# Optimization experiments

Hardware: AMD Instinct MI355X
Metric: run time of the kernel (lower is better)

## Reference

```python
import jax, jax.numpy as jnp
import numpy as np

N_NODES = 100000
N_EDGES = 1600000
IN_CH = 128
HID = 64
HEADS = 4
N_GRAPHS = 64
NEG_SLOPE = 0.2
LN_EPS = 1e-5


def setup_inputs() -> dict:
    key = jax.random.key(0)
    ks = jax.random.split(key, 24)
    C1 = HID // HEADS  # 16 per-head channels for conv1
    inp = {
        "x": jax.random.normal(ks[0], (N_NODES, IN_CH), dtype=jnp.float32),
        "edge_index": jax.random.randint(ks[1], (2, N_EDGES), 0, N_NODES, dtype=jnp.int64),
        "batch": jnp.sort(jax.random.randint(ks[2], (N_NODES,), 0, N_GRAPHS, dtype=jnp.int64)),
        "num_graphs": N_GRAPHS,
        # conv1: GATConv(IN_CH -> C1, heads=HEADS, concat)
        "W1": jax.random.normal(ks[3], (IN_CH, HEADS * C1), dtype=jnp.float32) * 0.05,
        "att_src1": jax.random.normal(ks[4], (HEADS, C1), dtype=jnp.float32) * 0.1,
        "att_dst1": jax.random.normal(ks[5], (HEADS, C1), dtype=jnp.float32) * 0.1,
        "b1": jnp.zeros((HEADS * C1,), dtype=jnp.float32),
        # conv2: GATConv(HID -> HID, heads=1)
        "W2": jax.random.normal(ks[6], (HID, HID), dtype=jnp.float32) * 0.1,
        "att_src2": jax.random.normal(ks[7], (1, HID), dtype=jnp.float32) * 0.1,
        "att_dst2": jax.random.normal(ks[8], (1, HID), dtype=jnp.float32) * 0.1,
        "b2": jnp.zeros((HID,), dtype=jnp.float32),
        "ln_g": jnp.ones((HID,), dtype=jnp.float32),
        "ln_b": jnp.zeros((HID,), dtype=jnp.float32),
        "w_pool": jax.random.normal(ks[9], (HID, 1), dtype=jnp.float32) * 0.1,
        "b_pool": jnp.zeros((1,), dtype=jnp.float32),
        "w_fc1": jax.random.normal(ks[10], (HID, HID), dtype=jnp.float32) * 0.1,
        "b_fc1": jnp.zeros((HID,), dtype=jnp.float32),
        "w_fc2": jax.random.normal(ks[11], (HID, 1), dtype=jnp.float32) * 0.1,
        "b_fc2": jnp.zeros((1,), dtype=jnp.float32),
    }
    return inp


def gat_conv(x, src, dst, n_nodes, W, att_src, att_dst, bias, heads, out_ch):
    """PyG GATConv (add_self_loops already folded into src/dst)."""
    h = (x @ W).reshape(n_nodes, heads, out_ch)         # [N,H,C]
    a_s = jnp.sum(h * att_src[None], axis=-1)           # [N,H]
    a_d = jnp.sum(h * att_dst[None], axis=-1)           # [N,H]
    alpha = jax.nn.leaky_relu(a_s[src] + a_d[dst], NEG_SLOPE)  # [E,H]
    amax = jax.ops.segment_max(alpha, dst, num_segments=n_nodes)
    amax = jnp.where(jnp.isfinite(amax), amax, 0.0)
    ex = jnp.exp(alpha - amax[dst])
    denom = jax.ops.segment_sum(ex, dst, num_segments=n_nodes)
    w = ex / (denom[dst] + 1e-16)                       # segment softmax over in-edges
    msg = h[src] * w[:, :, None]                        # [E,H,C]
    out = jax.ops.segment_sum(msg, dst, num_segments=n_nodes)
    return out.reshape(n_nodes, heads * out_ch) + bias


def reference(x, edge_index, batch, num_graphs, W1, att_src1, att_dst1, b1,
              W2, att_src2, att_dst2, b2, ln_g, ln_b, w_pool, b_pool,
              w_fc1, b_fc1, w_fc2, b_fc2):
    n = x.shape[0]
    loop = jnp.arange(n, dtype=edge_index.dtype)
    src = jnp.concatenate([edge_index[0], loop])
    dst = jnp.concatenate([edge_index[1], loop])

    h = gat_conv(x, src, dst, n, W1, att_src1, att_dst1, b1, HEADS, HID // HEADS)
    h = jax.nn.elu(h)                                   # dropout is identity in eval
    h_res = h
    h = gat_conv(h, src, dst, n, W2, att_src2, att_dst2, b2, 1, HID)
    h = h + h_res
    mu = jnp.mean(h, axis=-1, keepdims=True)
    var = jnp.mean(jnp.square(h - mu), axis=-1, keepdims=True)
    h = (h - mu) / jnp.sqrt(var + LN_EPS) * ln_g + ln_b
    h = jax.nn.elu(h)

    attn = jax.nn.softmax(h @ w_pool + b_pool, axis=0)  # softmax over ALL nodes (dim=0)
    pooled = jax.ops.segment_sum(h * attn, batch, num_segments=num_graphs)  # [G,HID]
    z = jax.nn.elu(pooled @ w_fc1 + b_fc1)
    return z @ w_fc2 + b_fc2                            # [G,1]
```

## Files before the change

kernel.cpp:

```cpp
#include <hip/hip_runtime.h>
#include <math.h>

#define NN 100000
#define NE 1600000
#define ICH 128
#define HID 64
#define NGR 64
#define NB_SCAN 391

__device__ __forceinline__ float lrelu(float x){ return x > 0.f ? x : 0.2f*x; }
__device__ __forceinline__ float eluf(float x){ return x > 0.f ? x : expm1f(x); }

__device__ __forceinline__ float bf2f(unsigned short u){
  return __uint_as_float(((unsigned int)u) << 16);
}
__device__ __forceinline__ unsigned short f2bf(float f){
  unsigned int u = __float_as_uint(f);
  return (unsigned short)((u + 0x7FFF + ((u >> 16) & 1)) >> 16);
}

__device__ __forceinline__ float wsum64(float v){
  #pragma unroll
  for (int m = 32; m >= 1; m >>= 1) v += __shfl_xor(v, m);
  return v;
}
__device__ __forceinline__ float wsum16(float v){
  v += __shfl_xor(v, 8); v += __shfl_xor(v, 4);
  v += __shfl_xor(v, 2); v += __shfl_xor(v, 1);
  return v;
}
__device__ __forceinline__ int wscan_incl(int v){
  const int lane = threadIdx.x & 63;
  #pragma unroll
  for (int d = 1; d < 64; d <<= 1){
    int t = __shfl_up(v, d);
    if (lane >= d) v += t;
  }
  return v;
}

__global__ __launch_bounds__(256) void k_deg(const int* __restrict__ ei_dst,
                                             int* __restrict__ deg)
{
  const int lo = (blockIdx.x & 3) * 25000, hi = lo + 25000;
  const int nb = gridDim.x >> 2, ib = blockIdx.x >> 2;
  for (int e = ib * 256 + threadIdx.x; e < NE; e += nb * 256){
    int d = ei_dst[e];
    if (d >= lo && d < hi) atomicAdd(&deg[d], 1);
  }
}

__global__ __launch_bounds__(256) void k_scanA(const int* __restrict__ deg,
    int* __restrict__ rowptr, int* __restrict__ bsum)
{
  int i = blockIdx.x * 256 + threadIdx.x;
  int v = (i < NN) ? deg[i] : 0;
  int incl = wscan_incl(v);
  __shared__ int wsums[4];
  int w = threadIdx.x >> 6, lane = threadIdx.x & 63;
  if (lane == 63) wsums[w] = incl;
  __syncthreads();
  int off = 0;
  for (int k = 0; k < w; ++k) off += wsums[k];
  if (i < NN) rowptr[i] = incl - v + off;
  if (threadIdx.x == 255) bsum[blockIdx.x] = off + incl;
}

__global__ __launch_bounds__(512) void k_scanB(const int* __restrict__ bsum,
                                               int* __restrict__ boff)
{
  int i = threadIdx.x;
  int v = (i < NB_SCAN) ? bsum[i] : 0;
  int incl = wscan_incl(v);
  __shared__ int wsums[8];
  int w = threadIdx.x >> 6, lane = threadIdx.x & 63;
  if (lane == 63) wsums[w] = incl;
  __syncthreads();
  int off = 0;
  for (int k = 0; k < w; ++k) off += wsums[k];
  if (i < NB_SCAN) boff[i] = incl - v + off;
}

__global__ __launch_bounds__(256) void k_scanC(int* __restrict__ rowptr,
    const int* __restrict__ boff, int* __restrict__ cursor)
{
  int i = blockIdx.x * 256 + threadIdx.x;
  if (i < NN){
    int val = rowptr[i] + boff[blockIdx.x];
    rowptr[i] = val;
    cursor[i] = val;
  }
  if (i == 0) rowptr[NN] = NE;
}

__global__ __launch_bounds__(256) void k_scatter(const int* __restrict__ ei,
    int* __restrict__ cursor, int* __restrict__ csr_src)
{
  const int lo = (blockIdx.x & 7) * 12500, hi = lo + 12500;
  const int nb = gridDim.x >> 3, ib = blockIdx.x >> 3;
  for (int e = ib * 256 + threadIdx.x; e < NE; e += nb * 256){
    int d = ei[NE + e];
    if (d >= lo && d < hi){
      int pos = atomicAdd(&cursor[d], 1);
      csr_src[pos] = ei[e];
    }
  }
}

__global__ __launch_bounds__(256) void k_gemm1(const float* __restrict__ x,
    const float* __restrict__ W1, const float* __restrict__ asw,
    const float* __restrict__ adw, unsigned short* __restrict__ h1b,
    float* __restrict__ as1, float* __restrict__ ad1)
{
  __shared__ float xs[16 * ICH];
  const int t = threadIdx.x;
  const int n0 = blockIdx.x * 16;
  const float4* xg4 = (const float4*)(x + (size_t)n0 * ICH);
  float4* xs4 = (float4*)xs;
  xs4[t]       = xg4[t];
  xs4[t + 256] = xg4[t + 256];
  __syncthreads();

  const int lane = t & 63;
  const float* xr = xs + (t >> 6) * 4 * ICH;
  float a0 = 0.f, a1 = 0.f, a2 = 0.f, a3 = 0.f;
  #pragma unroll 8
  for (int k = 0; k < ICH; ++k){
    const float w = W1[k * HID + lane];
    a0 = fmaf(xr[k],          w, a0);
    a1 = fmaf(xr[ICH + k],    w, a1);
    a2 = fmaf(xr[2*ICH + k],  w, a2);
    a3 = fmaf(xr[3*ICH + k],  w, a3);
  }
  const float sw = asw[lane], dw = adw[lane];
  const int nw = n0 + (t >> 6) * 4;
  float acc[4] = {a0, a1, a2, a3};
  #pragma unroll
  for (int i = 0; i < 4; ++i){
    const int n = nw + i;
    h1b[(size_t)n * HID + lane] = f2bf(acc[i]);
    float ps = wsum16(acc[i] * sw);
    float pd = wsum16(acc[i] * dw);
    if ((lane & 15) == 0){
      as1[n * 4 + (lane >> 4)] = ps;
      ad1[n * 4 + (lane >> 4)] = pd;
    }
  }
}

__global__ __launch_bounds__(256) void k_conv1(const int* __restrict__ rowptr,
    const int* __restrict__ csr_src, const float* __restrict__ as1,
    const float* __restrict__ ad1, const unsigned short* __restrict__ h1b,
    const float* __restrict__ b1, float* __restrict__ hb)
{
  const int lane = threadIdx.x & 63;
  const int h = lane >> 4;
  const int n = (blockIdx.x * 256 + threadIdx.x) >> 6;
  const int row0 = __builtin_amdgcn_readfirstlane(rowptr[n]);
  const int row1 = __builtin_amdgcn_readfirstlane(rowptr[n + 1]);
  const float adh = ad1[4 * n + h];
  float eh = __expf(lrelu(as1[4 * n + h] + adh));
  float den = eh;
  float acc = eh * bf2f(h1b[(size_t)n * HID + lane]);
  #pragma unroll 4
  for (int j = row0; j < row1; ++j){
    int s = csr_src[j];
    float e = __expf(lrelu(as1[4 * s + h] + adh));
    den += e;
    acc = fmaf(bf2f(h1b[(size_t)s * HID + lane]), e, acc);
  }
  float o = acc / (den + 1e-16f) + b1[lane];
  hb[(size_t)n * HID + lane] = eluf(o);
}

__global__ __launch_bounds__(256) void k_gemm2(const float* __restrict__ h,
    const float* __restrict__ W2, const float* __restrict__ asw,
    const float* __restrict__ adw, unsigned short* __restrict__ h2b,
    float* __restrict__ as2, float* __restrict__ ad2)
{
  __shared__ float hs[16 * HID];
  const int t = threadIdx.x;
  const int n0 = blockIdx.x * 16;
  const float4* hg4 = (const float4*)(h + (size_t)n0 * HID);
  float4* hs4 = (float4*)hs;
  hs4[t] = hg4[t];
  __syncthreads();

  const int lane = t & 63;
  const float* hr = hs + (t >> 6) * 4 * HID;
  float a0 = 0.f, a1 = 0.f, a2 = 0.f, a3 = 0.f;
  #pragma unroll 8
  for (int k = 0; k < HID; ++k){
    const float w = W2[k * HID + lane];
    a0 = fmaf(hr[k],          w, a0);
    a1 = fmaf(hr[HID + k],    w, a1);
    a2 = fmaf(hr[2*HID + k],  w, a2);
    a3 = fmaf(hr[3*HID + k],  w, a3);
  }
  const float sw = asw[lane], dw = adw[lane];
  const int nw = n0 + (t >> 6) * 4;
  float acc[4] = {a0, a1, a2, a3};
  #pragma unroll
  for (int i = 0; i < 4; ++i){
    const int n = nw + i;
    h2b[(size_t)n * HID + lane] = f2bf(acc[i]);
    float ps = wsum64(acc[i] * sw);
    float pd = wsum64(acc[i] * dw);
    if (lane == 0){ as2[n] = ps; ad2[n] = pd; }
  }
}

__global__ __launch_bounds__(256) void k_conv2(const int* __restrict__ rowptr,
    const int* __restrict__ csr_src, const float* __restrict__ as2,
    const float* __restrict__ ad2, const unsigned short* __restrict__ h2b,
    const float* __restrict__ b2, float* __restrict__ hb,
    const float* __restrict__ lng, const float* __restrict__ lnb,
    const float* __restrict__ wpool, const float* __restrict__ bpool,
    float* __restrict__ es)
{
  const int lane = threadIdx.x & 63;
  const int n = (blockIdx.x * 256 + threadIdx.x) >> 6;
  const int row0 = __builtin_amdgcn_readfirstlane(rowptr[n]);
  const int row1 = __builtin_amdgcn_readfirstlane(rowptr[n + 1]);
  const float adn = ad2[n];
  float eh = __expf(lrelu(as2[n] + adn));
  float den = eh;
  float acc = eh * bf2f(h2b[(size_t)n * HID + lane]);
  #pragma unroll 4
  for (int j = row0; j < row1; ++j){
    int s = csr_src[j];
    float e = __expf(lrelu(as2[s] + adn));
    den += e;
    acc = fmaf(bf2f(h2b[(size_t)s * HID + lane]), e, acc);
  }
  const size_t idxn = (size_t)n * HID + lane;
  float t = acc / (den + 1e-16f) + b2[lane] + hb[idxn];
  float mu  = wsum64(t) * (1.f / 64.f);
  float dv  = t - mu;
  float var = wsum64(dv * dv) * (1.f / 64.f);
  float hv = dv * (1.f / sqrtf(var + 1e-5f)) * lng[lane] + lnb[lane];
  hv = eluf(hv);
  hb[idxn] = hv;
  float sl = wsum64(hv * wpool[lane]) + bpool[0];
  if (lane == 0) es[n] = __expf(sl);
}

__global__ __launch_bounds__(256) void k_sumes(const float* __restrict__ es,
                                               float* __restrict__ S)
{
  float v = 0.f;
  for (int i = blockIdx.x * 256 + threadIdx.x; i < NN; i += gridDim.x * 256)
    v += es[i];
  v = wsum64(v);
  __shared__ float red[4];
  if ((threadIdx.x & 63) == 0) red[threadIdx.x >> 6] = v;
  __syncthreads();
  if (threadIdx.x == 0) atomicAdd(S, red[0] + red[1] + red[2] + red[3]);
}

__global__ __launch_bounds__(256) void k_pool(const float* __restrict__ hf,
    const float* __restrict__ es, const int* __restrict__ batch,
    const float* __restrict__ S, float* __restrict__ pooled)
{
  const int lane = threadIdx.x & 63;
  const int wseg = blockIdx.x * 4 + (threadIdx.x >> 6);
  const int base = wseg * 64;
  if (base >= NN) return;
  const float invS = 1.f / S[0];
  int end = base + 64; if (end > NN) end = NN;
  float acc = 0.f;
  int gprev = batch[base];
  for (int n = base; n < end; ++n){
    int g = batch[n];
    if (g != gprev){
      atomicAdd(&pooled[gprev * HID + lane], acc);
      acc = 0.f; gprev = g;
    }
    acc = fmaf(hf[(size_t)n * HID + lane], es[n] * invS, acc);
  }
  atomicAdd(&pooled[gprev * HID + lane], acc);
}

__global__ __launch_bounds__(64) void k_head(const float* __restrict__ pooled,
    const float* __restrict__ wfc1, const float* __restrict__ bfc1,
    const float* __restrict__ wfc2, const float* __restrict__ bfc2,
    float* __restrict__ out)
{
  const int g = blockIdx.x, j = threadIdx.x;
  const float* pr = pooled + g * HID;
  float acc = bfc1[j];
  #pragma unroll 4
  for (int k = 0; k < HID; ++k) acc = fmaf(pr[k], wfc1[k * HID + j], acc);
  float z = eluf(acc);
  float r = wsum64(z * wfc2[j]);
  if (j == 0) out[g] = r + bfc2[0];
}

extern "C" void kernel_launch(void* const* d_in, const int* in_sizes, int n_in,
                              void* d_out, int out_size, void* d_ws, size_t ws_size,
                              hipStream_t stream)
{
  const float* x     = (const float*)d_in[0];
  const int*   ei    = (const int*)d_in[1];
  const int*   batch = (const int*)d_in[2];
  const float* W1    = (const float*)d_in[4];
  const float* asw1  = (const float*)d_in[5];
  const float* adw1  = (const float*)d_in[6];
  const float* b1    = (const float*)d_in[7];
  const float* W2    = (const float*)d_in[8];
  const float* asw2  = (const float*)d_in[9];
  const float* adw2  = (const float*)d_in[10];
  const float* b2    = (const float*)d_in[11];
  const float* lng   = (const float*)d_in[12];
  const float* lnb   = (const float*)d_in[13];
  const float* wpool = (const float*)d_in[14];
  const float* bpool = (const float*)d_in[15];
  const float* wfc1  = (const float*)d_in[16];
  const float* bfc1  = (const float*)d_in[17];
  const float* wfc2  = (const float*)d_in[18];
  const float* bfc2  = (const float*)d_in[19];

  float* ws = (float*)d_ws;
  float* hb     = ws;
  float* as1    = ws +  6400000;
  float* ad1    = ws +  6800000;
  float* as2    = ws +  7200000;
  float* ad2    = ws +  7300000;
  float* es     = ws +  7400000;
  float* pooled = ws +  7500000;
  float* Ssum   = ws +  7504096;
  unsigned short* hub = (unsigned short*)(ws + 7504100);
  int* iw       = (int*)(ws + 10704100);
  int* rowptr   = iw;
  int* cursor   = iw + 100004;
  int* deg      = iw + 200008;
  int* bsum     = iw + 300008;
  int* boff     = iw + 300520;
  int* csr_src  = iw + 301032;

  hipMemsetAsync(deg, 0, (size_t)NN * 4, stream);
  hipMemsetAsync(pooled, 0, (size_t)NGR * 64 * 4, stream);
  hipMemsetAsync(Ssum, 0, 4, stream);

  k_deg    <<<2048, 256, 0, stream>>>(ei + NE, deg);
  k_scanA  <<<NB_SCAN, 256, 0, stream>>>(deg, rowptr, bsum);
  k_scanB  <<<1, 512, 0, stream>>>(bsum, boff);
  k_scanC  <<<NB_SCAN, 256, 0, stream>>>(rowptr, boff, cursor);
  k_scatter<<<2048, 256, 0, stream>>>(ei, cursor, csr_src);

  k_gemm1<<<6250, 256, 0, stream>>>(x, W1, asw1, adw1, hub, as1, ad1);
  k_conv1<<<25000, 256, 0, stream>>>(rowptr, csr_src, as1, ad1, hub, b1, hb);
  k_gemm2<<<6250, 256, 0, stream>>>(hb, W2, asw2, adw2, hub, as2, ad2);
  k_conv2<<<25000, 256, 0, stream>>>(rowptr, csr_src, as2, ad2, hub, b2, hb,
                                     lng, lnb, wpool, bpool, es);
  k_sumes<<<128, 256, 0, stream>>>(es, Ssum);
  k_pool <<<391, 256, 0, stream>>>(hb, es, batch, Ssum, pooled);
  k_head <<<64, 64, 0, stream>>>(pooled, wfc1, bfc1, wfc2, bfc2, (float*)d_out);
}
```

Baseline: 405.1 us.

## Compute edge attention weights cooperatively across lanes and broadcast via LDS

```diff
diff --git a/kernel.cpp b/kernel.cpp
--- a/kernel.cpp
+++ b/kernel.cpp
@@ -153,24 +153,38 @@
     const float* __restrict__ ad1, const unsigned short* __restrict__ h1b,
     const float* __restrict__ b1, float* __restrict__ hb)
 {
-  const int lane = threadIdx.x & 63;
+  __shared__ float2 buf[256];
+  const int t = threadIdx.x;
+  const int lane = t & 63;
   const int h = lane >> 4;
-  const int n = (blockIdx.x * 256 + threadIdx.x) >> 6;
+  const int m = lane & 15;
+  const int woff = t & 192;
+  const int n = (blockIdx.x * 256 + t) >> 6;
   const int row0 = __builtin_amdgcn_readfirstlane(rowptr[n]);
   const int row1 = __builtin_amdgcn_readfirstlane(rowptr[n + 1]);
   const float adh = ad1[4 * n + h];
-  float eh = __expf(lrelu(as1[4 * n + h] + adh));
-  float den = eh;
-  float acc = eh * bf2f(h1b[(size_t)n * HID + lane]);
-  #pragma unroll 4
-  for (int j = row0; j < row1; ++j){
-    int s = csr_src[j];
-    float e = __expf(lrelu(as1[4 * s + h] + adh));
-    den += e;
-    acc = fmaf(bf2f(h1b[(size_t)s * HID + lane]), e, acc);
-  }
+  const float eself = __expf(lrelu(as1[4 * n + h] + adh));
+  float acc = eself * bf2f(h1b[((unsigned)n << 6) | lane]);
+  float den_p = 0.f;
+  const int rbase = woff + (lane & 48);
+  for (int base = row0; base < row1; base += 16){
+    const int cnt = min(16, row1 - base);
+    int s = 0; float e = 0.f;
+    if (m < cnt){
+      s = csr_src[base + m];
+      e = __expf(lrelu(as1[4 * s + h] + adh));
+    }
+    den_p += e;
+    buf[woff + lane] = make_float2(e, __int_as_float(s));
+    for (int j = 0; j < cnt; ++j){
+      float2 es = buf[rbase + j];
+      int sj = __float_as_int(es.y);
+      acc = fmaf(bf2f(h1b[((unsigned)sj << 6) | lane]), es.x, acc);
+    }
+  }
+  float den = wsum16(den_p) + eself;
   float o = acc / (den + 1e-16f) + b1[lane];
-  hb[(size_t)n * HID + lane] = eluf(o);
+  hb[((size_t)n << 6) | lane] = eluf(o);
 }
 
 __global__ __launch_bounds__(256) void k_gemm2(const float* __restrict__ h,
@@ -218,25 +232,37 @@
     const float* __restrict__ wpool, const float* __restrict__ bpool,
     float* __restrict__ es)
 {
-  const int lane = threadIdx.x & 63;
-  const int n = (blockIdx.x * 256 + threadIdx.x) >> 6;
+  __shared__ float2 buf[256];
+  const int t = threadIdx.x;
+  const int lane = t & 63;
+  const int woff = t & 192;
+  const int n = (blockIdx.x * 256 + t) >> 6;
   const int row0 = __builtin_amdgcn_readfirstlane(rowptr[n]);
   const int row1 = __builtin_amdgcn_readfirstlane(rowptr[n + 1]);
   const float adn = ad2[n];
-  float eh = __expf(lrelu(as2[n] + adn));
-  float den = eh;
-  float acc = eh * bf2f(h2b[(size_t)n * HID + lane]);
-  #pragma unroll 4
-  for (int j = row0; j < row1; ++j){
-    int s = csr_src[j];
-    float e = __expf(lrelu(as2[s] + adn));
-    den += e;
-    acc = fmaf(bf2f(h2b[(size_t)s * HID + lane]), e, acc);
-  }
-  const size_t idxn = (size_t)n * HID + lane;
-  float t = acc / (den + 1e-16f) + b2[lane] + hb[idxn];
-  float mu  = wsum64(t) * (1.f / 64.f);
-  float dv  = t - mu;
+  const float eself = __expf(lrelu(as2[n] + adn));
+  float acc = eself * bf2f(h2b[((unsigned)n << 6) | lane]);
+  float den_p = 0.f;
+  for (int base = row0; base < row1; base += 64){
+    const int cnt = min(64, row1 - base);
+    int s = 0; float e = 0.f;
+    if (lane < cnt){
+      s = csr_src[base + lane];
+      e = __expf(lrelu(as2[s] + adn));
+    }
+    den_p += e;
+    buf[woff + lane] = make_float2(e, __int_as_float(s));
+    for (int j = 0; j < cnt; ++j){
+      float2 esv = buf[woff + j];
+      int sj = __float_as_int(esv.y);
+      acc = fmaf(bf2f(h2b[((unsigned)sj << 6) | lane]), esv.x, acc);
+    }
+  }
+  float den = wsum64(den_p) + eself;
+  const size_t idxn = ((size_t)n << 6) | lane;
+  float tv = acc / (den + 1e-16f) + b2[lane] + hb[idxn];
+  float mu  = wsum64(tv) * (1.f / 64.f);
+  float dv  = tv - mu;
   float var = wsum64(dv * dv) * (1.f / 64.f);
   float hv = dv * (1.f / sqrtf(var + 1e-5f)) * lng[lane] + lnb[lane];
   hv = eluf(hv);
```

Measured after the change: 404.6 us. No clear change (-0.1%).
